# Kernel optimization log

Hardware: AMD Instinct MI355X
Metric: run time of the kernel (lower is better)

Reference implementation:

```python
import math
import jax, jax.numpy as jnp
import numpy as np


def _proj(x, w, b):
    # 1x1x1 Conv3d == pointwise channel matmul: (B,C,T,H,W) x (O,C) -> (B,O,T,H,W)
    return jnp.einsum('bcthw,oc->bothw', x, w) + b[None, :, None, None, None]


def setup_inputs() -> dict:
    key = jax.random.key(0)
    ks = jax.random.split(key, 16)
    B, C, T, H, W = 2, 64, 16, 14, 14
    CI = C // 2
    s_in = 1.0 / math.sqrt(C)
    s_out = 1.0 / math.sqrt(CI)
    inp = {'x': jax.random.normal(ks[0], (B, C, T, H, W), jnp.float32)}
    # QKV projections for spatial (s) and temporal (t) branches: (CI, C) weights
    pnames = ['qs', 'ks', 'vs', 'qt', 'kt', 'vt']
    for i, n in enumerate(pnames):
        inp['W' + n] = jax.random.normal(ks[1 + i], (CI, C), jnp.float32) * s_in
        inp['b' + n] = jax.random.normal(ks[7 + i], (CI,), jnp.float32) * 0.01
    # output projection W: (C, CI)
    inp['Ww'] = jax.random.normal(ks[13], (C, CI), jnp.float32) * s_out
    inp['bw'] = jax.random.normal(ks[14], (C,), jnp.float32) * 0.01
    return inp


def reference(x, Wqs, bqs, Wks, bks, Wvs, bvs, Wqt, bqt, Wkt, bkt, Wvt, bvt, Ww, bw):
    B, C, T, H, W = x.shape
    CI = Wqs.shape[0]
    N = CI * H * W  # flat dim after original's raw .view (mixes channel & spatial/time)
    scale = 1.0 / math.sqrt(T)

    # ---- spatial branch: .view(B, T, -1) raw reshape of (B,CI,T,H,W) ----
    qs = _proj(x, Wqs, bqs).reshape(B, T, N).transpose(0, 2, 1)   # (B,N,T)
    ks_ = _proj(x, Wks, bks).reshape(B, T, N)                     # (B,T,N)
    vs = _proj(x, Wvs, bvs).reshape(B, T, N).transpose(0, 2, 1)   # (B,N,T)
    attn_s = jax.nn.softmax(jnp.einsum('bnt,btm->bnm', qs, ks_) * scale, axis=-1)  # (B,N,N)
    ys = jnp.einsum('bnm,bmt->bnt', attn_s, vs)                   # (B,N,T)
    ys = ys.transpose(0, 2, 1).reshape(B, CI, T, H, W)

    # ---- temporal branch: .view(B, CI*H*W, -1) raw reshape ----
    qt = _proj(x, Wqt, bqt).reshape(B, N, T).transpose(0, 2, 1)   # (B,T,N)
    kt = _proj(x, Wkt, bkt).reshape(B, N, T)                      # (B,N,T)
    vt = _proj(x, Wvt, bvt).reshape(B, N, T).transpose(0, 2, 1)   # (B,T,N)
    attn_t = jax.nn.softmax(jnp.einsum('btn,bns->bts', qt, kt) * scale, axis=-1)  # (B,T,T)
    yt = jnp.einsum('bts,bsn->btn', attn_t, vt)                   # (B,T,N)
    yt = yt.transpose(0, 2, 1).reshape(B, CI, T, H, W)

    y = ys + yt
    return _proj(y, Ww, bw) + x
```

## Files before the change

### kernel.cpp

```cpp
#include <hip/hip_runtime.h>
#include <math.h>

#define S3   3136
#define PB   100352
#define XB   200704
#define NN   6272
#define MW   7
#define MPW  896
#define TGC  49

typedef __attribute__((ext_vector_type(8))) short bf16x8;
typedef __attribute__((ext_vector_type(4))) float f32x4;

__device__ inline ushort f2bf(float f) {
    uint u = __float_as_uint(f);
    return (ushort)((u + 0x7FFFu + ((u >> 16) & 1u)) >> 16);
}

__global__ __launch_bounds__(256) void proj_kernel(
    const float* __restrict__ x,
    const float* __restrict__ W0, const float* __restrict__ b0,
    const float* __restrict__ W1, const float* __restrict__ b1,
    const float* __restrict__ W2, const float* __restrict__ b2,
    const float* __restrict__ W3, const float* __restrict__ b3,
    const float* __restrict__ W4, const float* __restrict__ b4,
    const float* __restrict__ W5, const float* __restrict__ b5,
    ushort* __restrict__ Qb, ushort* __restrict__ Kb, ushort* __restrict__ Vb,
    float* __restrict__ Qt, float* __restrict__ Kt, float* __restrict__ Vt)
{
    const float* Wp; const float* bp;
    switch (blockIdx.y) {
        case 0:  Wp = W0; bp = b0; break;
        case 1:  Wp = W1; bp = b1; break;
        case 2:  Wp = W2; bp = b2; break;
        case 3:  Wp = W3; bp = b3; break;
        case 4:  Wp = W4; bp = b4; break;
        default: Wp = W5; bp = b5; break;
    }
    int z = blockIdx.z;

    int gid = blockIdx.x * 256 + threadIdx.x;
    if (gid >= 2 * S3) return;
    int b = (gid >= S3) ? 1 : 0;
    int s = gid - b * S3;

    float xr[64];
    #pragma unroll
    for (int c = 0; c < 64; ++c) xr[c] = x[(size_t)b * XB + (size_t)c * S3 + s];

    float a[16];
    #pragma unroll
    for (int oo = 0; oo < 16; ++oo) {
        int o = z * 16 + oo;
        float acc = bp[o];
        #pragma unroll
        for (int c = 0; c < 64; ++c) acc = fmaf(Wp[o * 64 + c], xr[c], acc);
        a[oo] = acc;
    }

    if (blockIdx.y < 2) {
        const float sc = (blockIdx.y == 0) ? 0.36067376022224085f : 1.0f;
        ushort* ob = (blockIdx.y == 0) ? Qb : Kb;
        #pragma unroll
        for (int h = 0; h < 2; ++h) {
            int n = h * S3 + s;
            uint u0 = f2bf(a[0 + h] * sc)  | ((uint)f2bf(a[2 + h]  * sc) << 16);
            uint u1 = f2bf(a[4 + h] * sc)  | ((uint)f2bf(a[6 + h]  * sc) << 16);
            uint u2 = f2bf(a[8 + h] * sc)  | ((uint)f2bf(a[10 + h] * sc) << 16);
            uint u3 = f2bf(a[12 + h] * sc) | ((uint)f2bf(a[14 + h] * sc) << 16);
            *(uint4*)(ob + ((size_t)(b * NN + n) * 16 + z * 8)) = make_uint4(u0, u1, u2, u3);
        }
    } else if (blockIdx.y == 2) {
        #pragma unroll
        for (int oo = 0; oo < 16; ++oo) {
            int o = z * 16 + oo;
            Vb[(size_t)(b * 16 + (o >> 1)) * NN + (o & 1) * S3 + s] = f2bf(a[oo]);
        }
    } else {
        float* op = (blockIdx.y == 3) ? Qt : (blockIdx.y == 4) ? Kt : Vt;
        #pragma unroll
        for (int oo = 0; oo < 16; ++oo)
            op[(size_t)b * PB + (size_t)(z * 16 + oo) * S3 + s] = a[oo];
    }
}

__global__ __launch_bounds__(256) void attn_kernel(
    const ushort* __restrict__ Qb, const ushort* __restrict__ Kb,
    const ushort* __restrict__ Vb, const float* __restrict__ Qt,
    const float* __restrict__ Kt,
    float* __restrict__ Pacc, float* __restrict__ Pl, float* __restrict__ Gp)
{
    __shared__ ushort ptile[4][16 * 40];
    __shared__ float qs[128 * 16], ks[128 * 16];

    int b = blockIdx.y;

    if (blockIdx.x >= 686) {
        int c = blockIdx.x - 686;
        size_t base = (size_t)b * PB + (size_t)c * 2048;
        for (int i = threadIdx.x; i < 512; i += 256) {
            ((float4*)qs)[i] = ((const float4*)(Qt + base))[i];
            ((float4*)ks)[i] = ((const float4*)(Kt + base))[i];
        }
        __syncthreads();
        int t = threadIdx.x >> 4, s = threadIdx.x & 15;
        float acc = 0.0f;
        #pragma unroll 8
        for (int n = 0; n < 128; ++n)
            acc = fmaf(qs[n * 16 + t], ks[n * 16 + s], acc);
        Gp[(size_t)(b * TGC + c) * 256 + threadIdx.x] = acc;
        return;
    }

    int wave = __builtin_amdgcn_readfirstlane((int)(threadIdx.x >> 6));
    int lane = threadIdx.x & 63;
    int col  = lane & 15;
    int kg   = lane >> 4;
    int gw   = blockIdx.x * 4 + wave;
    int ntile = gw / 7;
    int w     = gw - ntile * 7;
    int nbase = ntile * 16;
    int m0    = w * MPW;

    bf16x8 qf = {0, 0, 0, 0, 0, 0, 0, 0};
    if (kg < 2)
        qf = *(const bf16x8*)(Qb + ((size_t)(b * NN + nbase + col) * 16 + kg * 8));

    const bf16x8 ones = {16256, 16256, 16256, 16256, 16256, 16256, 16256, 16256};
    f32x4 zero4 = {0.f, 0.f, 0.f, 0.f};
    f32x4 yacc  = zero4;
    f32x4 lacc  = zero4;

    ushort* myt = ptile[wave];

    for (int it = 0; it < MPW / 32; ++it) {
        int mb = m0 + it * 32;
        bf16x8 vf = *(const bf16x8*)(Vb + ((size_t)(b * 16 + col) * NN + mb + kg * 8));

        #pragma unroll
        for (int tile = 0; tile < 2; ++tile) {
            int mt = mb + tile * 16;
            bf16x8 kf = {0, 0, 0, 0, 0, 0, 0, 0};
            if (kg < 2)
                kf = *(const bf16x8*)(Kb + ((size_t)(b * NN + mt + col) * 16 + kg * 8));
            f32x4 st = __builtin_amdgcn_mfma_f32_16x16x32_bf16(kf, qf, zero4, 0, 0, 0);
            float p0 = __builtin_amdgcn_exp2f(st[0]);
            float p1 = __builtin_amdgcn_exp2f(st[1]);
            float p2 = __builtin_amdgcn_exp2f(st[2]);
            float p3 = __builtin_amdgcn_exp2f(st[3]);
            uint lo = f2bf(p0) | ((uint)f2bf(p1) << 16);
            uint hi = f2bf(p2) | ((uint)f2bf(p3) << 16);
            *(uint2*)(myt + (col * 40 + tile * 16 + kg * 4)) = make_uint2(lo, hi);
        }
        bf16x8 pf = *(bf16x8*)(myt + (col * 40 + kg * 8));
        yacc = __builtin_amdgcn_mfma_f32_16x16x32_bf16(vf, pf, yacc, 0, 0, 0);
        lacc = __builtin_amdgcn_mfma_f32_16x16x32_bf16(ones, pf, lacc, 0, 0, 0);
    }

    #pragma unroll
    for (int r = 0; r < 4; ++r) {
        int t = kg * 4 + r;
        Pacc[((size_t)(b * 16 + t) * MW + w) * NN + nbase + col] = yacc[r];
    }
    if (kg == 0)
        Pl[((size_t)b * MW + w) * NN + nbase + col] = lacc[0];
}

__global__ __launch_bounds__(256) void merge_final(
    const float* __restrict__ Pacc, const float* __restrict__ Pl,
    const float* __restrict__ Gp, const float* __restrict__ Vt,
    const float* __restrict__ x, const float* __restrict__ Ww,
    const float* __restrict__ bw, float* __restrict__ out)
{
    __shared__ float Lsh[256];
    __shared__ float Ash[16][17];
    __shared__ float Wsh[64 * 36];
    __shared__ float Ysh[16 * 36];

    int b  = blockIdx.y;
    int sc = blockIdx.x;

    {
        float a = 0.0f;
        for (int c = 0; c < TGC; ++c)
            a += Gp[(size_t)(b * TGC + c) * 256 + threadIdx.x];
        Lsh[threadIdx.x] = a * 0.25f;
        for (int i = threadIdx.x; i < 2048; i += 256)
            Wsh[(i >> 5) * 36 + (i & 31)] = Ww[i];
    }
    __syncthreads();
    if (threadIdx.x < 16) {
        int t = threadIdx.x;
        const float* Lr = &Lsh[t * 16];
        float mx = -1e30f;
        #pragma unroll
        for (int s = 0; s < 16; ++s) mx = fmaxf(mx, Lr[s]);
        float e[16]; float sm = 0.0f;
        #pragma unroll
        for (int s = 0; s < 16; ++s) { e[s] = __expf(Lr[s] - mx); sm += e[s]; }
        float inv = 1.0f / sm;
        #pragma unroll
        for (int s = 0; s < 16; ++s) Ash[s][t] = e[s] * inv;
    }
    __syncthreads();

    #pragma unroll
    for (int k = 0; k < 2; ++k) {
        int idx = threadIdx.x + k * 256;
        int ss = idx & 15;
        int ci = idx >> 4;
        int s  = sc * 16 + ss;
        int t  = ci >> 1;
        int nn = (ci & 1) * S3 + s;

        float a = 0.0f, l = 0.0f;
        #pragma unroll
        for (int w = 0; w < MW; ++w) {
            a += Pacc[((size_t)(b * 16 + t) * MW + w) * NN + nn];
            l += Pl[((size_t)b * MW + w) * NN + nn];
        }
        float ys = a / l;

        int t2 = nn & 15;
        const float4* vp = (const float4*)(Vt + (size_t)b * PB + (size_t)t * NN + (nn & ~15));
        float4 v0 = vp[0], v1 = vp[1], v2 = vp[2], v3 = vp[3];
        float yt = Ash[0][t2] * v0.x;
        yt = fmaf(Ash[1][t2],  v0.y, yt); yt = fmaf(Ash[2][t2],  v0.z, yt);
        yt = fmaf(Ash[3][t2],  v0.w, yt); yt = fmaf(Ash[4][t2],  v1.x, yt);
        yt = fmaf(Ash[5][t2],  v1.y, yt); yt = fmaf(Ash[6][t2],  v1.z, yt);
        yt = fmaf(Ash[7][t2],  v1.w, yt); yt = fmaf(Ash[8][t2],  v2.x, yt);
        yt = fmaf(Ash[9][t2],  v2.y, yt); yt = fmaf(Ash[10][t2], v2.z, yt);
        yt = fmaf(Ash[11][t2], v2.w, yt); yt = fmaf(Ash[12][t2], v3.x, yt);
        yt = fmaf(Ash[13][t2], v3.y, yt); yt = fmaf(Ash[14][t2], v3.z, yt);
        yt = fmaf(Ash[15][t2], v3.w, yt);

        Ysh[ss * 36 + ci] = ys + yt;
    }
    __syncthreads();

    int ss = threadIdx.x & 15;
    int cg = threadIdx.x >> 4;
    int s  = sc * 16 + ss;

    float acc[4];
    #pragma unroll
    for (int k = 0; k < 4; ++k) acc[k] = bw[cg * 4 + k];

    #pragma unroll
    for (int cb = 0; cb < 32; cb += 4) {
        float4 y4 = *(const float4*)&Ysh[ss * 36 + cb];
        #pragma unroll
        for (int k = 0; k < 4; ++k) {
            float4 w4 = *(const float4*)&Wsh[(cg * 4 + k) * 36 + cb];
            acc[k] = fmaf(w4.x, y4.x, acc[k]);
            acc[k] = fmaf(w4.y, y4.y, acc[k]);
            acc[k] = fmaf(w4.z, y4.z, acc[k]);
            acc[k] = fmaf(w4.w, y4.w, acc[k]);
        }
    }

    #pragma unroll
    for (int k = 0; k < 4; ++k) {
        int c = cg * 4 + k;
        size_t o = (size_t)b * XB + (size_t)c * S3 + s;
        out[o] = x[o] + acc[k];
    }
}

extern "C" void kernel_launch(void* const* d_in, const int* in_sizes, int n_in,
                              void* d_out, int out_size, void* d_ws, size_t ws_size,
                              hipStream_t stream)
{
    const float* x   = (const float*)d_in[0];
    const float* Wqs = (const float*)d_in[1];  const float* bqs = (const float*)d_in[2];
    const float* Wks = (const float*)d_in[3];  const float* bks = (const float*)d_in[4];
    const float* Wvs = (const float*)d_in[5];  const float* bvs = (const float*)d_in[6];
    const float* Wqt = (const float*)d_in[7];  const float* bqt = (const float*)d_in[8];
    const float* Wkt = (const float*)d_in[9];  const float* bkt = (const float*)d_in[10];
    const float* Wvt = (const float*)d_in[11]; const float* bvt = (const float*)d_in[12];
    const float* Ww  = (const float*)d_in[13]; const float* bw  = (const float*)d_in[14];

    float* ws = (float*)d_ws;
    ushort* Qb = (ushort*)(ws);
    ushort* Kb = (ushort*)(ws + 100352);
    ushort* Vb = (ushort*)(ws + 200704);
    float* Qt  = ws + 301056;
    float* Kt  = ws + 501760;
    float* Vt  = ws + 702464;
    float* Gp  = ws + 903168;
    float* Pacc = ws + 928256;
    float* Pl   = ws + 2333184;

    proj_kernel<<<dim3(25, 6, 2), 256, 0, stream>>>(
        x, Wqs, bqs, Wks, bks, Wvs, bvs, Wqt, bqt, Wkt, bkt, Wvt, bvt,
        Qb, Kb, Vb, Qt, Kt, Vt);

    attn_kernel<<<dim3(686 + TGC, 2), 256, 0, stream>>>(
        Qb, Kb, Vb, Qt, Kt, Pacc, Pl, Gp);

    merge_final<<<dim3(196, 2), 256, 0, stream>>>(
        Pacc, Pl, Gp, Vt, x, Ww, bw, (float*)d_out);
}
```

Baseline: 141.2 us.

## Switch spatial attention to 32x32x16 MFMA with register-resident P via permlane swap

Rewrites the spatial attention inner loop to use 32x32x16 bf16 MFMA tiles. The exponentiated score matrix is repacked in registers with v_cvt_pk_bf16_f32 and v_permlane32_swap instead of a round trip through LDS. The row-sum is folded into the PV MFMA by putting a ones row into the V operand, which removes the separate lacc MFMA. The M range is split across 14 partitions instead of 7, which doubles the partial buffers that merge_final must reduce. Correctness depends on the lane layout of the swap matching the MFMA operand layout, and merge_final (not shown) must agree with MW=14.

```diff
diff --git a/kernel.cpp b/kernel.cpp
--- a/kernel.cpp
+++ b/kernel.cpp
@@ -5,16 +5,28 @@
 #define PB   100352
 #define XB   200704
 #define NN   6272
-#define MW   7
-#define MPW  896
+#define MW   14
+#define MPW  448
 #define TGC  49
 
 typedef __attribute__((ext_vector_type(8))) short bf16x8;
 typedef __attribute__((ext_vector_type(4))) float f32x4;
+typedef __attribute__((ext_vector_type(16))) float f32x16;
+typedef __attribute__((ext_vector_type(4))) uint u32x4;
 
 __device__ inline ushort f2bf(float f) {
     uint u = __float_as_uint(f);
     return (ushort)((u + 0x7FFFu + ((u >> 16) & 1u)) >> 16);
+}
+
+__device__ inline uint cvtpk(float lo, float hi) {
+    uint r;
+    asm("v_cvt_pk_bf16_f32 %0, %1, %2" : "=v"(r) : "v"(lo), "v"(hi));
+    return r;
+}
+
+__device__ inline void swap32(uint &a, uint &b) {
+    asm("v_permlane32_swap_b32 %0, %1" : "+v"(a), "+v"(b));
 }
 
 __global__ __launch_bounds__(256) void proj_kernel(
@@ -90,7 +102,6 @@
     const float* __restrict__ Kt,
     float* __restrict__ Pacc, float* __restrict__ Pl, float* __restrict__ Gp)
 {
-    __shared__ ushort ptile[4][16 * 40];
     __shared__ float qs[128 * 16], ks[128 * 16];
 
     int b = blockIdx.y;
@@ -114,56 +125,60 @@
 
     int wave = __builtin_amdgcn_readfirstlane((int)(threadIdx.x >> 6));
     int lane = threadIdx.x & 63;
-    int col  = lane & 15;
-    int kg   = lane >> 4;
+    int col  = lane & 31;
+    int h    = lane >> 5;
     int gw   = blockIdx.x * 4 + wave;
-    int ntile = gw / 7;
-    int w     = gw - ntile * 7;
-    int nbase = ntile * 16;
+    int ntile = gw / 14;
+    int w     = gw - ntile * 14;
+    int nbase = ntile * 32;
     int m0    = w * MPW;
 
-    bf16x8 qf = {0, 0, 0, 0, 0, 0, 0, 0};
-    if (kg < 2)
-        qf = *(const bf16x8*)(Qb + ((size_t)(b * NN + nbase + col) * 16 + kg * 8));
-
-    const bf16x8 ones = {16256, 16256, 16256, 16256, 16256, 16256, 16256, 16256};
-    f32x4 zero4 = {0.f, 0.f, 0.f, 0.f};
-    f32x4 yacc  = zero4;
-    f32x4 lacc  = zero4;
-
-    ushort* myt = ptile[wave];
+    bf16x8 qf = *(const bf16x8*)(Qb + ((size_t)(b * NN + nbase + col) * 16 + h * 8));
+
+    const bf16x8 vzero = {0, 0, 0, 0, 0, 0, 0, 0};
+    const bf16x8 vones = {16256, 16256, 16256, 16256, 16256, 16256, 16256, 16256};
+    f32x16 yacc;
+    #pragma unroll
+    for (int r = 0; r < 16; ++r) yacc[r] = 0.0f;
+    f32x16 zero16 = yacc;
 
     for (int it = 0; it < MPW / 32; ++it) {
         int mb = m0 + it * 32;
-        bf16x8 vf = *(const bf16x8*)(Vb + ((size_t)(b * 16 + col) * NN + mb + kg * 8));
-
-        #pragma unroll
-        for (int tile = 0; tile < 2; ++tile) {
-            int mt = mb + tile * 16;
-            bf16x8 kf = {0, 0, 0, 0, 0, 0, 0, 0};
-            if (kg < 2)
-                kf = *(const bf16x8*)(Kb + ((size_t)(b * NN + mt + col) * 16 + kg * 8));
-            f32x4 st = __builtin_amdgcn_mfma_f32_16x16x32_bf16(kf, qf, zero4, 0, 0, 0);
-            float p0 = __builtin_amdgcn_exp2f(st[0]);
-            float p1 = __builtin_amdgcn_exp2f(st[1]);
-            float p2 = __builtin_amdgcn_exp2f(st[2]);
-            float p3 = __builtin_amdgcn_exp2f(st[3]);
-            uint lo = f2bf(p0) | ((uint)f2bf(p1) << 16);
-            uint hi = f2bf(p2) | ((uint)f2bf(p3) << 16);
-            *(uint2*)(myt + (col * 40 + tile * 16 + kg * 4)) = make_uint2(lo, hi);
-        }
-        bf16x8 pf = *(bf16x8*)(myt + (col * 40 + kg * 8));
-        yacc = __builtin_amdgcn_mfma_f32_16x16x32_bf16(vf, pf, yacc, 0, 0, 0);
-        lacc = __builtin_amdgcn_mfma_f32_16x16x32_bf16(ones, pf, lacc, 0, 0, 0);
-    }
-
-    #pragma unroll
-    for (int r = 0; r < 4; ++r) {
-        int t = kg * 4 + r;
+        bf16x8 kf = *(const bf16x8*)(Kb + ((size_t)(b * NN + mb + col) * 16 + h * 8));
+        bf16x8 vf0 = vzero, vf1 = vzero;
+        if (col < 16) {
+            const ushort* vp = Vb + ((size_t)(b * 16 + col) * NN + mb + h * 8);
+            vf0 = *(const bf16x8*)(vp);
+            vf1 = *(const bf16x8*)(vp + 16);
+        } else if (col == 16) { vf0 = vones; vf1 = vones; }
+
+        f32x16 st = __builtin_amdgcn_mfma_f32_32x32x16_bf16(kf, qf, zero16, 0, 0, 0);
+        float pv[16];
+        #pragma unroll
+        for (int r = 0; r < 16; ++r) pv[r] = __builtin_amdgcn_exp2f(st[r]);
+
+        uint X0 = cvtpk(pv[0],  pv[1]),  X1 = cvtpk(pv[2],  pv[3]);
+        uint Y0 = cvtpk(pv[4],  pv[5]),  Y1 = cvtpk(pv[6],  pv[7]);
+        uint X2 = cvtpk(pv[8],  pv[9]),  X3 = cvtpk(pv[10], pv[11]);
+        uint Y2 = cvtpk(pv[12], pv[13]), Y3 = cvtpk(pv[14], pv[15]);
+        swap32(X0, Y0); swap32(X1, Y1);
+        swap32(X2, Y2); swap32(X3, Y3);
+        u32x4 pb0 = {X0, X1, Y0, Y1};
+        u32x4 pb1 = {X2, X3, Y2, Y3};
+
+        yacc = __builtin_amdgcn_mfma_f32_32x32x16_bf16(
+                   vf0, __builtin_bit_cast(bf16x8, pb0), yacc, 0, 0, 0);
+        yacc = __builtin_amdgcn_mfma_f32_32x32x16_bf16(
+                   vf1, __builtin_bit_cast(bf16x8, pb1), yacc, 0, 0, 0);
+    }
+
+    #pragma unroll
+    for (int r = 0; r < 8; ++r) {
+        int t = (r & 3) + 8 * (r >> 2) + 4 * h;
         Pacc[((size_t)(b * 16 + t) * MW + w) * NN + nbase + col] = yacc[r];
     }
-    if (kg == 0)
-        Pl[((size_t)b * MW + w) * NN + nbase + col] = lacc[0];
+    if (h == 0)
+        Pl[((size_t)b * MW + w) * NN + nbase + col] = yacc[8];
 }
 
 __global__ __launch_bounds__(256) void merge_final(
@@ -289,7 +304,7 @@
     float* Vt  = ws + 702464;
     float* Gp  = ws + 903168;
     float* Pacc = ws + 928256;
-    float* Pl   = ws + 2333184;
+    float* Pl   = ws + 3738112;
 
     proj_kernel<<<dim3(25, 6, 2), 256, 0, stream>>>(
         x, Wqs, bqs, Wks, bks, Wvs, bvs, Wqt, bqt, Wkt, bkt, Wvt, bvt,
```

Measured after the change: 131.6 us. 1.07x faster.
